# Kernel tuning notes

Measured on AMD Instinct MI355X. Metric: run time of the kernel, lower is better.

## Reference

```python
import jax, jax.numpy as jnp
import numpy as np

B, D_IN, H, D_OUT = 1024, 512, 512, 512


def _act(v):
    # torch.relu(x) ** 2
    r = jnp.maximum(v, 0.0)
    return r * r


def setup_inputs() -> dict:
    key = jax.random.key(0)
    ks = jax.random.split(key, 8)
    x = jax.random.normal(ks[0], (B, D_IN), dtype=jnp.float32)
    # input_to_hidden: Linear(D_IN, H)
    W_in = jax.random.normal(ks[1], (D_IN, H), dtype=jnp.float32) / np.sqrt(D_IN)
    b_in = jax.random.normal(ks[2], (H,), dtype=jnp.float32) * 0.01
    # hidden_to_hidden[i]: Linear(1, H-i-1). Pack into padded arrays [H-1, H]
    # where row i, column j is the weight feeding output index j (valid only j > i).
    W_hh = jax.random.normal(ks[3], (H - 1, H), dtype=jnp.float32) * 0.02
    b_hh = jax.random.normal(ks[4], (H - 1, H), dtype=jnp.float32) * 0.01
    # hidden_to_output: Linear(H, D_OUT)
    W_out = jax.random.normal(ks[5], (H, D_OUT), dtype=jnp.float32) / np.sqrt(H)
    b_out = jax.random.normal(ks[6], (D_OUT,), dtype=jnp.float32) * 0.01
    return {"x": x, "W_in": W_in, "b_in": b_in, "W_hh": W_hh, "b_hh": b_hh,
            "W_out": W_out, "b_out": b_out}


def reference(x, W_in, b_in, W_hh, b_hh, W_out, b_out):
    h0 = _act(x @ W_in + b_in)  # [B, H]
    hid = h0.shape[1]
    col = jnp.arange(hid)

    def step(h, inp):
        i, w, b = inp  # w, b: [H] padded rows
        src = jnp.take(h, i, axis=1)  # [B], uses UPDATED h (strict sequential dep)
        contrib = _act(src[:, None] * w[None, :] + b[None, :])  # [B, H]
        mask = (col > i).astype(h.dtype)  # only columns i+1.. get updated
        return h + contrib * mask[None, :], None

    xs = (jnp.arange(hid - 1), W_hh, b_hh)
    h, _ = jax.lax.scan(step, h0, xs)
    return h @ W_out + b_out  # [B, D_OUT]
```

## Files before the change

kernel.cpp:

```cpp
#include <hip/hip_runtime.h>

#define B_SZ 1024
#define DIN 512
#define HH 512
#define DOUT 512

typedef short bf16x8 __attribute__((ext_vector_type(8)));
typedef float f32x4 __attribute__((ext_vector_type(4)));

__device__ __forceinline__ unsigned short f2bf(float f) {
    unsigned int u = __float_as_uint(f);
    u += 0x7FFFu + ((u >> 16) & 1u);
    return (unsigned short)(u >> 16);
}
__device__ __forceinline__ float bf2f(unsigned short s) {
    return __uint_as_float(((unsigned int)s) << 16);
}

__device__ __forceinline__ uint4 cvt8(const float4& a0, const float4& a1, int term) {
    const float av[8] = {a0.x, a0.y, a0.z, a0.w, a1.x, a1.y, a1.z, a1.w};
    unsigned int p[4];
    #pragma unroll
    for (int q = 0; q < 4; ++q) {
        float f0 = av[2 * q], f1 = av[2 * q + 1];
        unsigned short h0 = f2bf(f0), h1 = f2bf(f1);
        if (term == 1) { h0 = f2bf(f0 - bf2f(h0)); h1 = f2bf(f1 - bf2f(h1)); }
        p[q] = (unsigned int)h0 | ((unsigned int)h1 << 16);
    }
    uint4 v; v.x = p[0]; v.y = p[1]; v.z = p[2]; v.w = p[3];
    return v;
}

__device__ __forceinline__ void gload_lds16(const void* g, void* l) {
    __builtin_amdgcn_global_load_lds(
        (__attribute__((address_space(1))) void*)g,
        (__attribute__((address_space(3))) void*)l, 16, 0, 0);
}

__device__ __forceinline__ void convW_body(const float* __restrict__ W,
                                           uint4* __restrict__ dst, int t) {
    const int lane = t & 63;
    const int fb   = t >> 6;
    const int ks   = fb >> 5;
    const int nf   = fb & 31;
    const int col  = nf * 16 + (lane & 15);
    const int kb   = ks * 32 + ((lane >> 4) << 3);
    const int term = kb >> 9;
    const int c0   = kb & 511;
    unsigned short o[8];
    #pragma unroll
    for (int j = 0; j < 8; ++j) {
        const float f = W[(size_t)(c0 + j) * 512 + col];
        unsigned short hi = f2bf(f);
        o[j] = (term == 2) ? f2bf(f - bf2f(hi)) : hi;
    }
    uint4 v;
    v.x = (unsigned int)o[0] | ((unsigned int)o[1] << 16);
    v.y = (unsigned int)o[2] | ((unsigned int)o[3] << 16);
    v.z = (unsigned int)o[4] | ((unsigned int)o[5] << 16);
    v.w = (unsigned int)o[6] | ((unsigned int)o[7] << 16);
    dst[t] = v;
}

template <int C>
__device__ __forceinline__ void pack_bulk(const float* __restrict__ W_hh,
                                          const float* __restrict__ b_hh,
                                          float2* __restrict__ wbk, int e) {
    constexpr int NK = 7 - C;
    constexpr int CB = (C==0?0:C==1?7:C==2?13:C==3?18:C==4?22:C==5?25:27) * 4096;
    const int s   = e / (NK * 64);
    const int rem = e - s * (NK * 64);
    const int row = 64 * C + s;
    const int col = 64 * (C + 1) + rem;
    float2 o;
    o.x = W_hh[(size_t)row * 512 + col];
    o.y = b_hh[(size_t)row * 512 + col];
    wbk[CB + e] = o;
}

__global__ __launch_bounds__(256)
void prep_all(const float* __restrict__ W_hh, const float* __restrict__ b_hh,
              float2* __restrict__ wdg, float2* __restrict__ wbk,
              const float* __restrict__ W_in, uint4* __restrict__ Bin,
              const float* __restrict__ W_out, uint4* __restrict__ Bout) {
    const int b = blockIdx.x;
    const int tid = threadIdx.x;
    if (b < 128) {
        const int idx = b * 256 + tid;
        const int i = idx >> 6, l = idx & 63;
        float2 o;
        if (i < 511 && l > (i & 63)) {
            const int col = ((i >> 6) << 6) + l;
            o.x = W_hh[(size_t)i * 512 + col];
            o.y = b_hh[(size_t)i * 512 + col];
        } else { o.x = 0.0f; o.y = -1.0f; }
        wdg[idx] = o;
    } else if (b < 576) {
        const int rb = b - 128;
        if      (rb < 112) pack_bulk<0>(W_hh, b_hh, wbk, (rb      ) * 256 + tid);
        else if (rb < 208) pack_bulk<1>(W_hh, b_hh, wbk, (rb - 112) * 256 + tid);
        else if (rb < 288) pack_bulk<2>(W_hh, b_hh, wbk, (rb - 208) * 256 + tid);
        else if (rb < 352) pack_bulk<3>(W_hh, b_hh, wbk, (rb - 288) * 256 + tid);
        else if (rb < 400) pack_bulk<4>(W_hh, b_hh, wbk, (rb - 352) * 256 + tid);
        else if (rb < 432) pack_bulk<5>(W_hh, b_hh, wbk, (rb - 400) * 256 + tid);
        else               pack_bulk<6>(W_hh, b_hh, wbk, (rb - 432) * 256 + tid);
    } else if (b < 960) {
        convW_body(W_in, Bin, (b - 576) * 256 + tid);
    } else {
        convW_body(W_out, Bout, (b - 960) * 256 + tid);
    }
}

template <bool ACT>
__global__ __launch_bounds__(512, 2)
void mfma_gemm(const float* __restrict__ A,
               const uint4* __restrict__ Bg,
               const float* __restrict__ bias,
               float* __restrict__ C) {
    __shared__ uint4 lds[2][768];
    const int tid  = threadIdx.x;
    const int lane = tid & 63;
    const int w    = tid >> 6;
    const int mfw  = w & 3;
    const int nfw  = w >> 2;
    const int mf0  = blockIdx.x * 4;
    const int nf0  = blockIdx.y * 2;

    const int ks_s = tid >> 8;
    const int mf_s = (tid >> 6) & 3;
    const int arow = (mf0 + mf_s) * 16 + (lane & 15);
    const int koff = (lane >> 4) << 3;
    const int bks  = tid >> 7;
    const int bnf  = (tid >> 6) & 1;

    float4 Ra0, Ra1; uint4 R2;
    auto stage = [&](int s) {
        const int kp = (s * 2 + ks_s) * 32 + koff;
        const int c  = kp & 511;
        Ra0 = *(const float4*)&A[(size_t)arow * 512 + c];
        Ra1 = *(const float4*)&A[(size_t)arow * 512 + c + 4];
        if (tid < 256)
            R2 = Bg[(size_t)((s * 2 + bks) * 32 + nf0 + bnf) * 64 + lane];
    };
    auto write_tile = [&](int buf, int s) {
        const int kp = (s * 2 + ks_s) * 32 + koff;
        lds[buf][ks_s * 256 + mf_s * 64 + lane] = cvt8(Ra0, Ra1, kp >> 9);
        if (tid < 256)
            lds[buf][512 + bks * 128 + bnf * 64 + lane] = R2;
    };

    f32x4 acc = {0.f, 0.f, 0.f, 0.f};

    stage(0);
    write_tile(0, 0);
    stage(1);
    __syncthreads();

    for (int s = 0; s < 24; ++s) {
        const int cur = s & 1;
        if (s + 1 < 24) write_tile(cur ^ 1, s + 1);
        if (s + 2 < 24) stage(s + 2);
        __builtin_amdgcn_sched_barrier(0);

        bf16x8 aF0 = *(const bf16x8*)&lds[cur][          mfw * 64 + lane];
        bf16x8 aF1 = *(const bf16x8*)&lds[cur][256     + mfw * 64 + lane];
        bf16x8 bF0 = *(const bf16x8*)&lds[cur][512     + nfw * 64 + lane];
        bf16x8 bF1 = *(const bf16x8*)&lds[cur][512+128 + nfw * 64 + lane];
        acc = __builtin_amdgcn_mfma_f32_16x16x32_bf16(aF0, bF0, acc, 0, 0, 0);
        acc = __builtin_amdgcn_mfma_f32_16x16x32_bf16(aF1, bF1, acc, 0, 0, 0);
        __syncthreads();
    }

    const int colg  = (nf0 + nfw) * 16 + (lane & 15);
    const float bv  = bias[colg];
    const int rbase = (mf0 + mfw) * 16 + ((lane >> 4) << 2);
    #pragma unroll
    for (int r = 0; r < 4; ++r) {
        float v = acc[r] + bv;
        if (ACT) { v = fmaxf(v, 0.f); v = v * v; }
        C[(size_t)(rbase + r) * 512 + colg] = v;
    }
}

template <int C>
__device__ __forceinline__ void scan_chunk(const float2* __restrict__ wdg,
                                           const float2* __restrict__ wbk,
                                           float2 (* __restrict__ smb)[3584],
                                           float (* __restrict__ comm)[64],
                                           float hrp[8], int lane, int row_l,
                                           int par, int tid) {
    constexpr int NK = 7 - C;
    constexpr int CB = (C==0?0:C==1?7:C==2?13:C==3?18:C==4?22:C==5?25:C==6?27:27) * 4096;

    const char* gch = (const char*)(wbk + CB);
    char* lbase = (char*)(&smb[0][0]) + ((tid >> 6) << 10);
    auto stage = [&](int t, int buf) {
        const char* g = gch + (size_t)t * (NK * 4096);
        char* l = lbase + buf * 28672;
        #pragma unroll
        for (int u = 0; u < NK; ++u)
            gload_lds16(g + (size_t)((u << 8) + tid) * 16, l + (u << 12));
    };
    if constexpr (NK > 0) stage(0, 0);
    __builtin_amdgcn_sched_barrier(0);

    if (par == 1) comm[row_l][lane] = hrp[C];
    __syncthreads();

    if (par == 0) {
        hrp[C] += comm[row_l][lane];
        const float2* dptr = wdg + (64 * C) * 64 + lane;
        float2 Wd[16];
        #pragma unroll
        for (int q = 0; q < 16; ++q) Wd[q] = dptr[q * 64];
        for (int t = 0; t < 4; ++t) {
            #pragma unroll
            for (int q = 0; q < 16; ++q) {
                const int s = t * 16 + q;
                if (!(C == 7 && s == 63)) {
                    const float hi = __uint_as_float(
                        __builtin_amdgcn_readlane(__float_as_uint(hrp[C]), s));
                    const float tv = fmaf(hi, Wd[q].x, Wd[q].y);
                    const float rv = fmaxf(tv, 0.f);
                    hrp[C] = fmaf(rv, rv, hrp[C]);
                }
                if (t < 3) Wd[q] = dptr[(s + 16) * 64];
            }
        }
        comm[row_l][lane] = hrp[C];
    }
    __syncthreads();

    if constexpr (NK > 0) {
        const float hsrc = (par == 0) ? hrp[C] : comm[row_l][lane];
        for (int t = 0; t < 8; ++t) {
            const int buf = t & 1;
            if (t + 1 < 8) stage(t + 1, buf ^ 1);
            __builtin_amdgcn_sched_barrier(0);

            #pragma unroll
            for (int sl = 0; sl < 4; ++sl) {
                const int srow = 2 * sl + par;
                const float hi = __uint_as_float(
                    __builtin_amdgcn_readlane(__float_as_uint(hsrc), t * 8 + srow));
                #pragma unroll
                for (int k = 0; k < NK; ++k) {
                    const float2 wv = smb[buf][(srow * NK + k) * 64 + lane];
                    const float tv = fmaf(hi, wv.x, wv.y);
                    const float rv = fmaxf(tv, 0.f);
                    hrp[C + 1 + k] = fmaf(rv, rv, hrp[C + 1 + k]);
                }
            }
            __syncthreads();
        }
    }
}

__global__ __launch_bounds__(256, 2)
void scan_kernel(const float2* __restrict__ wdg, const float2* __restrict__ wbk,
                 float* __restrict__ h) {
    __shared__ __align__(16) float2 smb[2][3584];
    __shared__ float comm[2][64];
    const int tid   = threadIdx.x;
    const int lane  = tid & 63;
    const int w     = tid >> 6;
    const int row_l = w & 1;
    const int par   = w >> 1;
    float* hrow = h + (size_t)(blockIdx.x * 2 + row_l) * HH;

    float hrp[8];
    #pragma unroll
    for (int k = 0; k < 8; ++k) hrp[k] = (par == 0) ? hrow[lane + 64 * k] : 0.f;

    scan_chunk<0>(wdg, wbk, smb, comm, hrp, lane, row_l, par, tid);
    scan_chunk<1>(wdg, wbk, smb, comm, hrp, lane, row_l, par, tid);
    scan_chunk<2>(wdg, wbk, smb, comm, hrp, lane, row_l, par, tid);
    scan_chunk<3>(wdg, wbk, smb, comm, hrp, lane, row_l, par, tid);
    scan_chunk<4>(wdg, wbk, smb, comm, hrp, lane, row_l, par, tid);
    scan_chunk<5>(wdg, wbk, smb, comm, hrp, lane, row_l, par, tid);
    scan_chunk<6>(wdg, wbk, smb, comm, hrp, lane, row_l, par, tid);
    scan_chunk<7>(wdg, wbk, smb, comm, hrp, lane, row_l, par, tid);

    if (par == 0) {
        #pragma unroll
        for (int k = 0; k < 8; ++k) hrow[lane + 64 * k] = hrp[k];
    }
}

extern "C" void kernel_launch(void* const* d_in, const int* in_sizes, int n_in,
                              void* d_out, int out_size, void* d_ws, size_t ws_size,
                              hipStream_t stream) {
    const float* x     = (const float*)d_in[0];
    const float* W_in  = (const float*)d_in[1];
    const float* b_in  = (const float*)d_in[2];
    const float* W_hh  = (const float*)d_in[3];
    const float* b_hh  = (const float*)d_in[4];
    const float* W_out = (const float*)d_in[5];
    const float* b_out = (const float*)d_in[6];
    float* out = (float*)d_out;

    char* ws = (char*)d_ws;
    float2* wdg  = (float2*)ws;
    float2* wbk  = (float2*)(ws + 0x040000u);
    float*  h    = (float*)(ws + 0x120000u);
    uint4*  Bin  = (uint4*)(ws + 0x320000u);
    uint4*  Bout = (uint4*)(ws + 0x4A0000u);

    prep_all<<<dim3(1344), dim3(256), 0, stream>>>(W_hh, b_hh, wdg, wbk,
                                                   W_in, Bin, W_out, Bout);

    mfma_gemm<true><<<dim3(16, 16), dim3(512), 0, stream>>>(x, Bin, b_in, h);

    scan_kernel<<<dim3(512), dim3(256), 0, stream>>>(wdg, wbk, h);

    mfma_gemm<false><<<dim3(16, 16), dim3(512), 0, stream>>>(h, Bout, b_out, out);
}
```

Baseline: 151.1 us.

## Per-wave private LDS ring buffer with vmcnt waits instead of block barriers in scan

Repacks the off-diagonal hidden weights by parity so each wave loads only the rows it consumes, staged into a private 4-slot LDS ring with global_load_lds. Block-wide __syncthreads in the bulk loop are replaced by per-wave s_waitcnt vmcnt waits, with three stages in flight. This removes inter-wave barrier stalls and halves redundant staging. In exchange it uses more LDS (64KB), which may limit the two-blocks-per-CU occupancy, and it depends on hand-counted vmcnt values being correct.

```diff
diff --git a/kernel.cpp b/kernel.cpp
--- a/kernel.cpp
+++ b/kernel.cpp
@@ -36,6 +36,12 @@
         (__attribute__((address_space(1))) void*)g,
         (__attribute__((address_space(3))) void*)l, 16, 0, 0);
 }
+
+template <int N>
+__device__ __forceinline__ void waitcnt_vm() {
+    asm volatile("s_waitcnt vmcnt(%0)" :: "n"(N) : "memory");
+}
+__device__ __forceinline__ void SB() { __builtin_amdgcn_sched_barrier(0); }
 
 __device__ __forceinline__ void convW_body(const float* __restrict__ W,
                                            uint4* __restrict__ dst, int t) {
@@ -68,10 +74,14 @@
                                           float2* __restrict__ wbk, int e) {
     constexpr int NK = 7 - C;
     constexpr int CB = (C==0?0:C==1?7:C==2?13:C==3?18:C==4?22:C==5?25:27) * 4096;
-    const int s   = e / (NK * 64);
-    const int rem = e - s * (NK * 64);
-    const int row = 64 * C + s;
-    const int col = 64 * (C + 1) + rem;
+    const int par = e / (2048 * NK);
+    const int r1  = e - par * (2048 * NK);
+    const int t   = r1 / (64 * NK);
+    const int r2  = r1 - t * (64 * NK);
+    const int k   = r2 >> 6;
+    const int l   = r2 & 63;
+    const int row = 64 * C + 2 * t + par;
+    const int col = 64 * (C + 1 + k) + l;
     float2 o;
     o.x = W_hh[(size_t)row * 512 + col];
     o.y = b_hh[(size_t)row * 512 + col];
@@ -184,28 +194,31 @@
 
 template <int C>
 __device__ __forceinline__ void scan_chunk(const float2* __restrict__ wdg,
-                                           const float2* __restrict__ wbk,
-                                           float2 (* __restrict__ smb)[3584],
+                                           const char* __restrict__ wbk,
+                                           char* __restrict__ myLds,
                                            float (* __restrict__ comm)[64],
                                            float hrp[8], int lane, int row_l,
-                                           int par, int tid) {
+                                           int par) {
     constexpr int NK = 7 - C;
-    constexpr int CB = (C==0?0:C==1?7:C==2?13:C==3?18:C==4?22:C==5?25:C==6?27:27) * 4096;
-
-    const char* gch = (const char*)(wbk + CB);
-    char* lbase = (char*)(&smb[0][0]) + ((tid >> 6) << 10);
-    auto stage = [&](int t, int buf) {
-        const char* g = gch + (size_t)t * (NK * 4096);
-        char* l = lbase + buf * 28672;
+    constexpr int CB = (C==0?0:C==1?7:C==2?13:C==3?18:C==4?22:C==5?25:C==6?27:27) * 32768;
+    constexpr int U  = (NK + 1) / 2;
+    constexpr int TB = NK * 512;
+    const char* gch = wbk + CB + par * (32 * TB);
+
+    auto stage = [&](int t) {
+        const char* g = gch + t * TB;
+        char* l = myLds + ((t & 3) << 12);
         #pragma unroll
-        for (int u = 0; u < NK; ++u)
-            gload_lds16(g + (size_t)((u << 8) + tid) * 16, l + (u << 12));
+        for (int u = 0; u < U; ++u)
+            gload_lds16(g + (u << 10) + lane * 16, l + (u << 10));
     };
-    if constexpr (NK > 0) stage(0, 0);
-    __builtin_amdgcn_sched_barrier(0);
+    if constexpr (NK > 0) { stage(0); stage(1); stage(2); }
+    SB();
 
     if (par == 1) comm[row_l][lane] = hrp[C];
-    __syncthreads();
+    asm volatile("s_waitcnt lgkmcnt(0)" ::: "memory");
+    __builtin_amdgcn_s_barrier();
+    SB();
 
     if (par == 0) {
         hrp[C] += comm[row_l][lane];
@@ -229,37 +242,42 @@
         }
         comm[row_l][lane] = hrp[C];
     }
-    __syncthreads();
+    asm volatile("s_waitcnt lgkmcnt(0)" ::: "memory");
+    __builtin_amdgcn_s_barrier();
+    SB();
 
     if constexpr (NK > 0) {
         const float hsrc = (par == 0) ? hrp[C] : comm[row_l][lane];
-        for (int t = 0; t < 8; ++t) {
-            const int buf = t & 1;
-            if (t + 1 < 8) stage(t + 1, buf ^ 1);
-            __builtin_amdgcn_sched_barrier(0);
-
+        const float2* lf = (const float2*)myLds;
+
+        auto compute = [&](int t) {
+            const float hi = __uint_as_float(__builtin_amdgcn_readlane(
+                __float_as_uint(hsrc), 2 * t + par));
             #pragma unroll
-            for (int sl = 0; sl < 4; ++sl) {
-                const int srow = 2 * sl + par;
-                const float hi = __uint_as_float(
-                    __builtin_amdgcn_readlane(__float_as_uint(hsrc), t * 8 + srow));
-                #pragma unroll
-                for (int k = 0; k < NK; ++k) {
-                    const float2 wv = smb[buf][(srow * NK + k) * 64 + lane];
-                    const float tv = fmaf(hi, wv.x, wv.y);
-                    const float rv = fmaxf(tv, 0.f);
-                    hrp[C + 1 + k] = fmaf(rv, rv, hrp[C + 1 + k]);
-                }
+            for (int k = 0; k < NK; ++k) {
+                const float2 wv = lf[((t & 3) << 9) + (k << 6) + lane];
+                const float tv = fmaf(hi, wv.x, wv.y);
+                const float rv = fmaxf(tv, 0.f);
+                hrp[C + 1 + k] = fmaf(rv, rv, hrp[C + 1 + k]);
             }
-            __syncthreads();
+        };
+        #pragma unroll 4
+        for (int t = 0; t < 28; ++t) {
+            waitcnt_vm<2 * U>(); SB();
+            compute(t);
+            stage(t + 3); SB();
         }
+        waitcnt_vm<2 * U>(); SB(); compute(28); stage(31); SB();
+        waitcnt_vm<2 * U>(); SB(); compute(29);
+        waitcnt_vm<U>();     SB(); compute(30);
+        waitcnt_vm<0>();     SB(); compute(31);
     }
 }
 
 __global__ __launch_bounds__(256, 2)
 void scan_kernel(const float2* __restrict__ wdg, const float2* __restrict__ wbk,
                  float* __restrict__ h) {
-    __shared__ __align__(16) float2 smb[2][3584];
+    __shared__ __align__(16) char smb[4][16384];
     __shared__ float comm[2][64];
     const int tid   = threadIdx.x;
     const int lane  = tid & 63;
@@ -272,14 +290,17 @@
     #pragma unroll
     for (int k = 0; k < 8; ++k) hrp[k] = (par == 0) ? hrow[lane + 64 * k] : 0.f;
 
-    scan_chunk<0>(wdg, wbk, smb, comm, hrp, lane, row_l, par, tid);
-    scan_chunk<1>(wdg, wbk, smb, comm, hrp, lane, row_l, par, tid);
-    scan_chunk<2>(wdg, wbk, smb, comm, hrp, lane, row_l, par, tid);
-    scan_chunk<3>(wdg, wbk, smb, comm, hrp, lane, row_l, par, tid);
-    scan_chunk<4>(wdg, wbk, smb, comm, hrp, lane, row_l, par, tid);
-    scan_chunk<5>(wdg, wbk, smb, comm, hrp, lane, row_l, par, tid);
-    scan_chunk<6>(wdg, wbk, smb, comm, hrp, lane, row_l, par, tid);
-    scan_chunk<7>(wdg, wbk, smb, comm, hrp, lane, row_l, par, tid);
+    char* myLds = &smb[w][0];
+    const char* wb = (const char*)wbk;
+
+    scan_chunk<0>(wdg, wb, myLds, comm, hrp, lane, row_l, par);
+    scan_chunk<1>(wdg, wb, myLds, comm, hrp, lane, row_l, par);
+    scan_chunk<2>(wdg, wb, myLds, comm, hrp, lane, row_l, par);
+    scan_chunk<3>(wdg, wb, myLds, comm, hrp, lane, row_l, par);
+    scan_chunk<4>(wdg, wb, myLds, comm, hrp, lane, row_l, par);
+    scan_chunk<5>(wdg, wb, myLds, comm, hrp, lane, row_l, par);
+    scan_chunk<6>(wdg, wb, myLds, comm, hrp, lane, row_l, par);
+    scan_chunk<7>(wdg, wb, myLds, comm, hrp, lane, row_l, par);
 
     if (par == 0) {
         #pragma unroll
```

Result: slower. 166.3 us (+10.1%).
